# Kernel optimization log

Measured on AMD Instinct MI355X. Metric: run time of the kernel, lower is better.

Reference implementation:

```python
import jax, jax.numpy as jnp
import numpy as np

B, T, DIM = 4, 2048, 2048
H = 16
Q_LORA, KV_LORA = 1536, 512
ROPE_D, NOPE_D, V_D = 64, 128, 128
Q_HEAD_D = NOPE_D + ROPE_D  # 192
EPS = 1e-6
ROPE_THETA = 500000.0


def rmsnorm(x, w):
    xf = x.astype(jnp.float32)
    rms = jax.lax.rsqrt(jnp.mean(xf * xf, axis=-1, keepdims=True) + EPS)
    return (xf * rms).astype(x.dtype) * w


def apply_rope(x, cos, sin):
    # x: (B,T,H,d); cos/sin: (T,d//2). Complex mult on interleaved pairs.
    d = x.shape[-1]
    xp = x.reshape(*x.shape[:-1], d // 2, 2)
    x0, x1 = xp[..., 0], xp[..., 1]
    c = cos[None, :, None, :]
    s = sin[None, :, None, :]
    o0 = x0 * c - x1 * s
    o1 = x0 * s + x1 * c
    return jnp.stack([o0, o1], axis=-1).reshape(x.shape)


def setup_inputs() -> dict:
    key = jax.random.key(0)
    ks = jax.random.split(key, 8)
    x = jax.random.normal(ks[0], (B, T, DIM), dtype=jnp.float32)
    # RoPE freqs as in standard precompute_freqs_cis
    inv_freq = 1.0 / (ROPE_THETA ** (np.arange(0, ROPE_D, 2, dtype=np.float32) / ROPE_D))
    t = np.arange(T, dtype=np.float32)
    ang = np.outer(t, inv_freq)  # (T, 32)
    freqs_cos = jnp.asarray(np.cos(ang))
    freqs_sin = jnp.asarray(np.sin(ang))
    # causal additive mask (1,1,T,T)
    mask = jnp.where(jnp.tril(jnp.ones((T, T), dtype=bool)), 0.0, -1e9).astype(jnp.float32)[None, None]
    sc = lambda fan_in: 1.0 / np.sqrt(fan_in)
    q_down_w = jax.random.normal(ks[1], (Q_LORA, DIM), dtype=jnp.float32) * sc(DIM)
    q_norm_w = jnp.ones((Q_LORA,), dtype=jnp.float32)
    q_up_nope_w = jax.random.normal(ks[2], (H * NOPE_D, Q_LORA), dtype=jnp.float32) * sc(Q_LORA)
    q_up_rope_w = jax.random.normal(ks[3], (H * ROPE_D, Q_LORA), dtype=jnp.float32) * sc(Q_LORA)
    kv_down_w = jax.random.normal(ks[4], (KV_LORA + ROPE_D, DIM), dtype=jnp.float32) * sc(DIM)
    kv_norm_w = jnp.ones((KV_LORA,), dtype=jnp.float32)
    kv_up_w = jax.random.normal(ks[5], (H * (NOPE_D + V_D), KV_LORA), dtype=jnp.float32) * sc(KV_LORA)
    wo_w = jax.random.normal(ks[6], (DIM, H * V_D), dtype=jnp.float32) * sc(H * V_D)
    return {"x": x, "freqs_cos": freqs_cos, "freqs_sin": freqs_sin, "mask": mask,
            "q_down_w": q_down_w, "q_norm_w": q_norm_w, "q_up_nope_w": q_up_nope_w,
            "q_up_rope_w": q_up_rope_w, "kv_down_w": kv_down_w, "kv_norm_w": kv_norm_w,
            "kv_up_w": kv_up_w, "wo_w": wo_w}


def reference(x, freqs_cos, freqs_sin, mask, q_down_w, q_norm_w, q_up_nope_w,
              q_up_rope_w, kv_down_w, kv_norm_w, kv_up_w, wo_w):
    b, t, _ = x.shape
    # Q path: low-rank down -> RMSNorm -> nope/rope up projections
    c_q = rmsnorm(x @ q_down_w.T, q_norm_w)                      # (B,T,q_lora)
    q_nope = (c_q @ q_up_nope_w.T).reshape(b, t, H, NOPE_D)
    q_rope = (c_q @ q_up_rope_w.T).reshape(b, t, H, ROPE_D)
    q_rope = apply_rope(q_rope, freqs_cos, freqs_sin)
    q = jnp.concatenate([q_nope, q_rope], axis=-1)               # (B,T,H,192)
    # KV path: shared low-rank latent + per-sequence rope key
    kv_raw = x @ kv_down_w.T                                     # (B,T,512+64)
    c_kv = kv_raw[..., :KV_LORA]
    k_rope = kv_raw[..., KV_LORA:][:, :, None, :]                # (B,T,1,64)
    k_rope = apply_rope(k_rope, freqs_cos, freqs_sin)
    k_rope = jnp.broadcast_to(k_rope, (b, t, H, ROPE_D))
    kv = (rmsnorm(c_kv, kv_norm_w) @ kv_up_w.T).reshape(b, t, H, NOPE_D + V_D)
    k_nope = kv[..., :NOPE_D]
    v = kv[..., NOPE_D:]                                         # (B,T,H,128)
    k = jnp.concatenate([k_nope, k_rope], axis=-1)               # (B,T,H,192)
    scale = Q_HEAD_D ** -0.5
    attn = jnp.einsum('bthd,bshd->bhts', q, k) * scale + mask    # (B,H,T,T)
    attn = jax.nn.softmax(attn, axis=-1)
    out = jnp.einsum('bhts,bshd->bthd', attn, v).reshape(b, t, H * V_D)
    return out @ wo_w.T
```

## Files before the change

### kernel.cpp

```cpp
#include <hip/hip_runtime.h>

#define BB 4
#define TT 2048
#define HH 16
#define ROWS (BB*TT)

typedef unsigned short u16;
typedef __bf16 bf16x8 __attribute__((ext_vector_type(8)));
typedef float f32x4 __attribute__((ext_vector_type(4)));
typedef u16 u16x8 __attribute__((ext_vector_type(8)));
typedef u16 u16x4 __attribute__((ext_vector_type(4)));

__device__ __forceinline__ u16 f2bf(float f) {
  unsigned u = __float_as_uint(f);
  u += 0x7fffu + ((u >> 16) & 1u);
  return (u16)(u >> 16);
}
__device__ __forceinline__ float bf2f(u16 h) {
  return __uint_as_float(((unsigned)h) << 16);
}

__device__ __forceinline__ void gload_lds16(const u16* g, u16* l) {
  __builtin_amdgcn_global_load_lds((const __attribute__((address_space(1))) void*)g,
                                   (__attribute__((address_space(3))) void*)l, 16, 0, 0);
}

__global__ __launch_bounds__(256) void cast_bf16(const float* __restrict__ in,
                                                 u16* __restrict__ out,
                                                 long n, float scale) {
  long i = ((long)blockIdx.x * 256 + threadIdx.x) * 4;
  long stride = (long)gridDim.x * 1024;
  for (; i < n; i += stride) {
    float4 v = *(const float4*)(in + i);
    u16x4 o = { f2bf(v.x*scale), f2bf(v.y*scale), f2bf(v.z*scale), f2bf(v.w*scale) };
    *(u16x4*)(out + i) = o;
  }
}

__global__ __launch_bounds__(256) void cast_pad(const float* __restrict__ in,
                                                u16* __restrict__ out,
                                                long n_in, long n_total) {
  long i = ((long)blockIdx.x * 256 + threadIdx.x) * 4;
  long stride = (long)gridDim.x * 1024;
  for (; i < n_total; i += stride) {
    u16x4 o;
    if (i + 3 < n_in) {
      float4 v = *(const float4*)(in + i);
      o = (u16x4){ f2bf(v.x), f2bf(v.y), f2bf(v.z), f2bf(v.w) };
    } else {
#pragma unroll
      for (int e = 0; e < 4; ++e) o[e] = (i + e < n_in) ? f2bf(in[i+e]) : (u16)0;
    }
    *(u16x4*)(out + i) = o;
  }
}

template<int OUT_BF16>
__global__ __launch_bounds__(512, 2) void gemm256(const u16* __restrict__ A,
                                                  const u16* __restrict__ Bm,
                                                  void* __restrict__ Cv,
                                                  int M, int N, int K, int lda) {
  __shared__ __align__(16) u16 lds[65536];
  const int tid = threadIdx.x;
  const int lane = tid & 63, wid = tid >> 6;
  const int wm = (wid >> 2) * 128;
  const int wn = (wid & 3) * 64;

  const int nx = gridDim.x;
  int id = blockIdx.y * nx + blockIdx.x;
  const int cpx = (nx * gridDim.y) >> 3;
  id = (id & 7) * cpx + (id >> 3);
  const int m0 = (id / nx) * 256;
  const int n0 = (id % nx) * 256;

  const int NT = K >> 6;

  f32x4 acc[8][4] = {};

  auto stage = [&](int kt, int d) {
#pragma unroll
    for (int j = 0; j < 4; ++j) {
      int c = j*512 + tid;
      int row = c >> 3;
      int colb = (c & 7) << 4;
      int srcb = colb ^ ((row & 7) << 4);
      const u16* ga = (const u16*)((const char*)A + ((long)(m0 + row) * lda + kt*64) * 2 + srcb);
      gload_lds16(ga, (u16*)((char*)lds + d*65536 + c*16));
      const u16* gb = (const u16*)((const char*)Bm + ((long)(n0 + row) * K + kt*64) * 2 + srcb);
      gload_lds16(gb, (u16*)((char*)lds + d*65536 + 32768 + c*16));
    }
  };

  stage(0, 0);
  stage(1, 1);

  const int lr = lane & 15;
  const int kb = (lane >> 4) << 4;

  for (int kt = 0; kt < NT; ++kt) {
    const int cur = kt & 1;
    if (kt + 1 < NT) asm volatile("s_waitcnt vmcnt(8)" ::: "memory");
    else             asm volatile("s_waitcnt vmcnt(0)" ::: "memory");
    __builtin_amdgcn_s_barrier();
    __builtin_amdgcn_sched_barrier(0);

    const char* Ab = (const char*)lds + cur*65536;
    const char* Bb = Ab + 32768;
#pragma unroll
    for (int qd = 0; qd < 4; ++qd) {
      const int mb = (qd >> 1) * 4;
      const int nb = (qd & 1) * 2;
      bf16x8 af[4][2], bf[2][2];
#pragma unroll
      for (int i = 0; i < 4; ++i) {
        int r = wm + (mb + i)*16 + lr;
#pragma unroll
        for (int ks = 0; ks < 2; ++ks)
          af[i][ks] = *(const bf16x8*)(Ab + r*128 + ((ks*64 + kb) ^ ((r & 7) << 4)));
      }
#pragma unroll
      for (int i = 0; i < 2; ++i) {
        int r = wn + (nb + i)*16 + lr;
#pragma unroll
        for (int ks = 0; ks < 2; ++ks)
          bf[i][ks] = *(const bf16x8*)(Bb + r*128 + ((ks*64 + kb) ^ ((r & 7) << 4)));
      }
      __builtin_amdgcn_s_setprio(1);
#pragma unroll
      for (int ks = 0; ks < 2; ++ks)
#pragma unroll
        for (int i = 0; i < 4; ++i)
#pragma unroll
          for (int j = 0; j < 2; ++j)
            acc[mb+i][nb+j] = __builtin_amdgcn_mfma_f32_16x16x32_bf16(af[i][ks], bf[j][ks], acc[mb+i][nb+j], 0, 0, 0);
      __builtin_amdgcn_s_setprio(0);
    }
    __builtin_amdgcn_sched_barrier(0);
    __builtin_amdgcn_s_barrier();
    if (kt + 2 < NT) stage(kt + 2, cur);
  }

  const int orow = (lane >> 4) << 2;
  const int ocol = lane & 15;
#pragma unroll
  for (int mf = 0; mf < 8; ++mf)
#pragma unroll
    for (int nf = 0; nf < 4; ++nf) {
      long rbase = (long)(m0 + wm + mf*16 + orow);
      int col = n0 + wn + nf*16 + ocol;
#pragma unroll
      for (int rr = 0; rr < 4; ++rr) {
        if (OUT_BF16) ((u16*)Cv)[(rbase + rr) * (long)N + col] = f2bf(acc[mf][nf][rr]);
        else          ((float*)Cv)[(rbase + rr) * (long)N + col] = acc[mf][nf][rr];
      }
    }
}

__global__ __launch_bounds__(256) void rmsnorm_bf(const u16* __restrict__ in, int istride,
                                                  const float* __restrict__ w,
                                                  u16* __restrict__ out, int ostride,
                                                  int N, float invn) {
  const long row = blockIdx.x;
  const u16* x = in + row * istride;
  u16* y = out + row * ostride;
  float ss = 0.f;
  for (int i = threadIdx.x * 8; i < N; i += 2048) {
    u16x8 v = *(const u16x8*)(x + i);
#pragma unroll
    for (int e = 0; e < 8; ++e) { float f = bf2f(v[e]); ss += f*f; }
  }
#pragma unroll
  for (int off = 32; off > 0; off >>= 1) ss += __shfl_down(ss, off);
  __shared__ float red[4];
  if ((threadIdx.x & 63) == 0) red[threadIdx.x >> 6] = ss;
  __syncthreads();
  float rms = rsqrtf((red[0]+red[1]+red[2]+red[3]) * invn + 1e-6f);
  for (int i = threadIdx.x * 8; i < N; i += 2048) {
    u16x8 v = *(const u16x8*)(x + i);
    u16x8 o;
#pragma unroll
    for (int e = 0; e < 8; ++e) o[e] = f2bf(bf2f(v[e]) * rms * w[i+e]);
    *(u16x8*)(y + i) = o;
  }
}

__global__ __launch_bounds__(256) void rope_qk(u16* __restrict__ qcat,
                                               const u16* __restrict__ dk,
                                               u16* __restrict__ Kr,
                                               const float* __restrict__ cosb,
                                               const float* __restrict__ sinb) {
  const int row = blockIdx.x;
  const int t = row & (TT-1);
  const float sc = 0.10411754661f;
  for (int p = threadIdx.x; p < 512; p += 256) {
    int h = p >> 5, i = p & 31;
    long base = (long)row*3072 + 2048 + h*64 + 2*i;
    float x0 = bf2f(qcat[base]), x1 = bf2f(qcat[base+1]);
    float c = cosb[t*32 + i], s = sinb[t*32 + i];
    qcat[base]   = f2bf((x0*c - x1*s)*sc);
    qcat[base+1] = f2bf((x0*s + x1*c)*sc);
  }
  if (threadIdx.x < 32) {
    int i = threadIdx.x;
    float x0 = bf2f(dk[(long)row*2304 + 2048 + 2*i]);
    float x1 = bf2f(dk[(long)row*2304 + 2048 + 2*i + 1]);
    float c = cosb[t*32 + i], s = sinb[t*32 + i];
    Kr[row*64 + 2*i]   = f2bf(x0*c - x1*s);
    Kr[row*64 + 2*i+1] = f2bf(x0*s + x1*c);
  }
}

__global__ __launch_bounds__(256) void transpose_v(const u16* __restrict__ kvb,
                                                   u16* __restrict__ Vt) {
  __shared__ u16 tile[64][136];
  const int bh = blockIdx.y;
  const int t0 = blockIdx.x << 6;
  const int tid = threadIdx.x;
  const long rowbase = (long)(bh >> 4) * TT + t0;
#pragma unroll
  for (int it = 0; it < 4; ++it) {
    int r = it*16 + (tid >> 4);
    int c = (tid & 15) << 3;
    u16x8 v = *(const u16x8*)(kvb + (rowbase + r) * 4096 + (bh & 15) * 256 + 128 + c);
#pragma unroll
    for (int e = 0; e < 8; ++e) tile[r][c+e] = v[e];
  }
  __syncthreads();
#pragma unroll
  for (int it = 0; it < 4; ++it) {
    int d = it*32 + (tid >> 3);
    int tc = (tid & 7) << 3;
    u16x8 o;
#pragma unroll
    for (int e = 0; e < 8; ++e) o[e] = tile[tc+e][d];
    *(u16x8*)(Vt + ((long)bh * 128 + d) * TT + t0 + tc) = o;
  }
}

__global__ __launch_bounds__(512) void flash_attn9(const u16* __restrict__ qcat,
                                                   const u16* __restrict__ kvb,
                                                   const u16* __restrict__ kr,
                                                   const u16* __restrict__ Vt,
                                                   u16* __restrict__ O) {
  __shared__ __align__(16) u16 lds[36864];
  const int bid = blockIdx.x;
  const int u = bid & 255, sl = bid >> 8;
  const int a = u >> 6;
  const int bh = u & 63;
  const int qt = sl ? a : (7 - a);
  const int b = bh >> 4, h = bh & 15;
  const int wid = threadIdx.x >> 6, lane = threadIdx.x & 63;
  const int q0 = qt*256 + wid*32;
  const long browq = (long)b * TT + q0;
  const long browk = (long)b * TT;
  const int l16 = lane >> 4;
  const int l8  = lane >> 3;
  const int lx16   = (lane & 15) * 16;
  const int lx8_16 = (lane & 7) * 16;
  const int co = l16 * 16;

  bf16x8 qf[2][6];
#pragma unroll
  for (int f = 0; f < 2; ++f) {
    long row = browq + f*16 + (lane & 15);
#pragma unroll
    for (int ks = 0; ks < 4; ++ks)
      qf[f][ks] = *(const bf16x8*)(qcat + row * 3072 + h*128 + ks*32 + l16 * 8);
#pragma unroll
    for (int ks = 0; ks < 2; ++ks)
      qf[f][4+ks] = *(const bf16x8*)(qcat + row * 3072 + 2048 + h*64 + ks*32 + l16 * 8);
  }

  bf16x8 vones;
#pragma unroll
  for (int e = 0; e < 8; ++e) vones[e] = (__bf16)1.0f;

  f32x4 oacc[2][8] = {};
  f32x4 lsum[2] = {};

  u16* pw = lds + 20480 + wid * 2048;

  const int nIter = 4*qt + 4;
  for (int it = 0; it < nIter; ++it) {
    const int s0 = it * 64;
#pragma unroll
    for (int j = 0; j < 2; ++j) {
      int c = j*8 + wid;
      int r = c*4 + l16;
      int cb = lx16 ^ ((r & 7) << 4);
      const u16* src = (const u16*)((const char*)kvb + (browk + s0 + r) * 8192 + h * 512 + cb);
      gload_lds16(src, lds + c*512);
    }
    {
      int c = wid;
      int r = c*8 + l8;
      int cb = lx8_16 ^ ((r & 7) << 4);
      const u16* src = (const u16*)((const char*)kr + (browk + s0 + r) * 128 + cb);
      gload_lds16(src, lds + 8192 + c*512);
    }
#pragma unroll
    for (int j = 0; j < 2; ++j) {
      int c = j*8 + wid;
      int d = c*8 + l8;
      int cb = lx8_16 ^ ((d & 7) << 4);
      const u16* src = (const u16*)((const char*)Vt + ((long)bh*128 + d) * (TT*2) + (long)s0*2 + cb);
      gload_lds16(src, lds + 12288 + c*512);
    }
    __syncthreads();

    const bool skip0 = s0 > q0 + 15;
    const bool skip1 = s0 > q0 + 31;
    if (!skip0 || !skip1) {
      __builtin_amdgcn_s_setprio(1);
      f32x4 sacc[2][4] = {};
#pragma unroll
      for (int nt = 0; nt < 4; ++nt) {
        const int r = nt*16 + (lane & 15);
        const int swz = (r & 7) << 4;
        bf16x8 kf[6];
#pragma unroll
        for (int ks = 0; ks < 4; ++ks)
          kf[ks] = *(const bf16x8*)((const char*)lds + r*256 + ((ks*64 + co) ^ swz));
#pragma unroll
        for (int ks = 0; ks < 2; ++ks)
          kf[4+ks] = *(const bf16x8*)((const char*)lds + 16384 + r*128 + ((ks*64 + co) ^ swz));
        if (!skip0) {
#pragma unroll
          for (int ks = 0; ks < 6; ++ks)
            sacc[0][nt] = __builtin_amdgcn_mfma_f32_16x16x32_bf16(qf[0][ks], kf[ks], sacc[0][nt], 0, 0, 0);
        }
        if (!skip1) {
#pragma unroll
          for (int ks = 0; ks < 6; ++ks)
            sacc[1][nt] = __builtin_amdgcn_mfma_f32_16x16x32_bf16(qf[1][ks], kf[ks], sacc[1][nt], 0, 0, 0);
        }
      }
#pragma unroll
      for (int f = 0; f < 2; ++f) {
        const bool skipf = f ? skip1 : skip0;
        if (skipf) continue;
        const int qmin = q0 + f*16;
        const int qb = qmin + (l16 << 2);
        if (s0 + 63 > qmin) {
#pragma unroll
          for (int nt = 0; nt < 4; ++nt) {
            int sc = s0 + nt*16 + (lane & 15);
#pragma unroll
            for (int rr = 0; rr < 4; ++rr)
              if (sc > qb + rr) sacc[f][nt][rr] = -1e30f;
          }
        }
        const int lb2 = (lane & 15) * 2;
#pragma unroll
        for (int rr = 0; rr < 4; ++rr) {
          float p0 = exp2f(sacc[f][0][rr] - 16.f);
          float p1 = exp2f(sacc[f][1][rr] - 16.f);
          float p2 = exp2f(sacc[f][2][rr] - 16.f);
          float p3 = exp2f(sacc[f][3][rr] - 16.f);
          const int prow = f*16 + (l16 << 2) + rr;
          const int sw = (prow & 7) << 4;
          char* pb = (char*)pw + prow*128;
          *(u16*)(pb + ((     lb2) ^ sw)) = f2bf(p0);
          *(u16*)(pb + (( 32 + lb2) ^ sw)) = f2bf(p1);
          *(u16*)(pb + (( 64 + lb2) ^ sw)) = f2bf(p2);
          *(u16*)(pb + (( 96 + lb2) ^ sw)) = f2bf(p3);
        }
      }
#pragma unroll
      for (int ks = 0; ks < 2; ++ks) {
        const int cb = ks*64 + co;
        bf16x8 vf[8];
#pragma unroll
        for (int vt = 0; vt < 8; ++vt) {
          int row = vt*16 + (lane & 15);
          vf[vt] = *(const bf16x8*)((const char*)lds + 24576 + row*128 + (cb ^ ((row & 7) << 4)));
        }
#pragma unroll
        for (int f = 0; f < 2; ++f) {
          if (f ? skip1 : skip0) continue;
          int prow = f*16 + (lane & 15);
          bf16x8 pa = *(const bf16x8*)((const char*)pw + prow*128 + (cb ^ ((prow & 7) << 4)));
          lsum[f] = __builtin_amdgcn_mfma_f32_16x16x32_bf16(pa, vones, lsum[f], 0, 0, 0);
#pragma unroll
          for (int vt = 0; vt < 8; ++vt)
            oacc[f][vt] = __builtin_amdgcn_mfma_f32_16x16x32_bf16(pa, vf[vt], oacc[f][vt], 0, 0, 0);
        }
      }
      __builtin_amdgcn_s_setprio(0);
    }
    __syncthreads();
  }

#pragma unroll
  for (int f = 0; f < 2; ++f) {
    float inv[4];
#pragma unroll
    for (int rr = 0; rr < 4; ++rr) inv[rr] = 1.f / lsum[f][rr];
#pragma unroll
    for (int vt = 0; vt < 8; ++vt)
#pragma unroll
      for (int rr = 0; rr < 4; ++rr) {
        long row = browq + f*16 + (l16 << 2) + rr;
        int col = h*128 + vt*16 + (lane & 15);
        O[row * 2048 + col] = f2bf(oacc[f][vt][rr] * inv[rr]);
      }
  }
}

static inline long minl(long a, long b) { return a < b ? a : b; }
static inline int cgrid(long n) { return (int)minl((n/4 + 255)/256, 4096L); }

extern "C" void kernel_launch(void* const* d_in, const int* in_sizes, int n_in,
                              void* d_out, int out_size, void* d_ws, size_t ws_size,
                              hipStream_t stream) {
  const float* x    = (const float*)d_in[0];
  const float* fcos = (const float*)d_in[1];
  const float* fsin = (const float*)d_in[2];
  const float* qdw  = (const float*)d_in[4];
  const float* qnw  = (const float*)d_in[5];
  const float* qunw = (const float*)d_in[6];
  const float* qurw = (const float*)d_in[7];
  const float* kvdw = (const float*)d_in[8];
  const float* kvnw = (const float*)d_in[9];
  const float* kvuw = (const float*)d_in[10];
  const float* wow  = (const float*)d_in[11];
  float* out = (float*)d_out;

  char* p = (char*)d_ws;
  auto alloc = [&](size_t bytes) { char* r = p; p += (bytes + 255) & ~(size_t)255; return r; };

  u16* xb   = (u16*)alloc((size_t)ROWS*2048*2);
  u16* wdc  = (u16*)alloc((size_t)2304*2048*2);
  u16* wuc  = (u16*)alloc((size_t)3072*1536*2);
  u16* wkvu = (u16*)alloc((size_t)4096*512*2);
  u16* wwo  = (u16*)alloc((size_t)2048*2048*2);
  u16* dk   = (u16*)alloc((size_t)ROWS*2304*2);
  u16* qcat = (u16*)alloc((size_t)ROWS*3072*2);
  u16* kvb  = (u16*)alloc((size_t)ROWS*4096*2);
  u16* kro  = (u16*)alloc((size_t)ROWS*64*2);

  u16* Vt = dk;
  u16* Ob = xb;

  const float QSC_E = 0.10411754661f;

  cast_bf16<<<cgrid((long)ROWS*2048), 256, 0, stream>>>(x, xb, (long)ROWS*2048, 1.f);
  cast_bf16<<<cgrid(1536L*2048), 256, 0, stream>>>(qdw, wdc, 1536L*2048, 1.f);
  cast_pad<<<cgrid(768L*2048), 256, 0, stream>>>(kvdw, wdc + 1536L*2048, 576L*2048, 768L*2048);
  cast_bf16<<<cgrid(2048L*1536), 256, 0, stream>>>(qunw, wuc, 2048L*1536, QSC_E);
  cast_bf16<<<cgrid(1024L*1536), 256, 0, stream>>>(qurw, wuc + 2048L*1536, 1024L*1536, 1.f);
  cast_bf16<<<cgrid(4096L*512), 256, 0, stream>>>(kvuw, wkvu, 4096L*512, 1.f);
  cast_bf16<<<cgrid(2048L*2048), 256, 0, stream>>>(wow, wwo, 2048L*2048, 1.f);

  gemm256<1><<<dim3(9, 32), 512, 0, stream>>>(xb, wdc, dk, ROWS, 2304, 2048, 2048);
  rmsnorm_bf<<<ROWS, 256, 0, stream>>>(dk, 2304, qnw, dk, 2304, 1536, 1.f/1536.f);
  rmsnorm_bf<<<ROWS, 256, 0, stream>>>(dk + 1536, 2304, kvnw, dk + 1536, 2304, 512, 1.f/512.f);
  gemm256<1><<<dim3(12, 32), 512, 0, stream>>>(dk, wuc, qcat, ROWS, 3072, 1536, 2304);
  gemm256<1><<<dim3(16, 32), 512, 0, stream>>>(dk + 1536, wkvu, kvb, ROWS, 4096, 512, 2304);
  rope_qk<<<ROWS, 256, 0, stream>>>(qcat, dk, kro, fcos, fsin);
  transpose_v<<<dim3(TT/64, BB*HH), 256, 0, stream>>>(kvb, Vt);
  flash_attn9<<<512, 512, 0, stream>>>(qcat, kvb, kro, Vt, Ob);
  gemm256<0><<<dim3(8, 32), 512, 0, stream>>>(Ob, wwo, out, ROWS, 2048, 2048, 2048);
}
```

Measured before the change: 575.0 us.

## Fuse weight casts, merge rmsnorm with k-rope, write V transposed from GEMM epilogue

Six weight-cast launches are merged into one multi-segment cast kernel. The two rmsnorms and the k-rope step are merged into a single per-row kernel. The kv-up GEMM now has an epilogue mode that writes k_nope to a compact buffer and V directly in transposed layout, which removes the separate transpose kernel and the full kvb round trip. Costs are fewer launches and less memory traffic, in exchange for 8-byte strided V stores in the epilogue and branchy segment selection in the cast kernel.

```diff
diff --git a/kernel.cpp b/kernel.cpp
--- a/kernel.cpp
+++ b/kernel.cpp
@@ -26,39 +26,57 @@
 }
 
 __global__ __launch_bounds__(256) void cast_bf16(const float* __restrict__ in,
-                                                 u16* __restrict__ out,
-                                                 long n, float scale) {
+                                                 u16* __restrict__ out, long n) {
   long i = ((long)blockIdx.x * 256 + threadIdx.x) * 4;
   long stride = (long)gridDim.x * 1024;
   for (; i < n; i += stride) {
     float4 v = *(const float4*)(in + i);
-    u16x4 o = { f2bf(v.x*scale), f2bf(v.y*scale), f2bf(v.z*scale), f2bf(v.w*scale) };
+    u16x4 o = { f2bf(v.x), f2bf(v.y), f2bf(v.z), f2bf(v.w) };
     *(u16x4*)(out + i) = o;
   }
 }
 
-__global__ __launch_bounds__(256) void cast_pad(const float* __restrict__ in,
-                                                u16* __restrict__ out,
-                                                long n_in, long n_total) {
+__global__ __launch_bounds__(256) void cast_weights(const float* __restrict__ qdw,
+                                                    const float* __restrict__ kvdw,
+                                                    const float* __restrict__ qunw,
+                                                    const float* __restrict__ qurw,
+                                                    const float* __restrict__ kvuw,
+                                                    const float* __restrict__ wow,
+                                                    u16* __restrict__ wdc,
+                                                    u16* __restrict__ wuc,
+                                                    u16* __restrict__ wkvu,
+                                                    u16* __restrict__ wwo,
+                                                    float qsc) {
+  const long s0 = 1536L*2048, s1 = 768L*2048, s2 = 2048L*1536,
+             s3 = 1024L*1536, s4 = 4096L*512,  s5 = 2048L*2048;
+  const long total = s0+s1+s2+s3+s4+s5;
   long i = ((long)blockIdx.x * 256 + threadIdx.x) * 4;
   long stride = (long)gridDim.x * 1024;
-  for (; i < n_total; i += stride) {
+  for (; i < total; i += stride) {
+    long off = i; const float* src; u16* dst; float sc = 1.f; long lim = -1;
+    if (off < s0)               { src = qdw;  dst = wdc; }
+    else if ((off -= s0) < s1)  { src = kvdw; dst = wdc + s0; lim = 576L*2048; }
+    else if ((off -= s1) < s2)  { src = qunw; dst = wuc; sc = qsc; }
+    else if ((off -= s2) < s3)  { src = qurw; dst = wuc + s2; }
+    else if ((off -= s3) < s4)  { src = kvuw; dst = wkvu; }
+    else { off -= s4;             src = wow;  dst = wwo; }
     u16x4 o;
-    if (i + 3 < n_in) {
-      float4 v = *(const float4*)(in + i);
-      o = (u16x4){ f2bf(v.x), f2bf(v.y), f2bf(v.z), f2bf(v.w) };
+    if (lim < 0 || off + 3 < lim) {
+      float4 v = *(const float4*)(src + off);
+      o = (u16x4){ f2bf(v.x*sc), f2bf(v.y*sc), f2bf(v.z*sc), f2bf(v.w*sc) };
     } else {
 #pragma unroll
-      for (int e = 0; e < 4; ++e) o[e] = (i + e < n_in) ? f2bf(in[i+e]) : (u16)0;
-    }
-    *(u16x4*)(out + i) = o;
-  }
-}
-
-template<int OUT_BF16>
+      for (int e = 0; e < 4; ++e) o[e] = (off + e < lim) ? f2bf(src[off+e]*sc) : (u16)0;
+    }
+    *(u16x4*)(dst + off) = o;
+  }
+}
+
+template<int MODE>
 __global__ __launch_bounds__(512, 2) void gemm256(const u16* __restrict__ A,
                                                   const u16* __restrict__ Bm,
                                                   void* __restrict__ Cv,
+                                                  u16* __restrict__ Vt,
                                                   int M, int N, int K, int lda) {
   __shared__ __align__(16) u16 lds[65536];
   const int tid = threadIdx.x;
@@ -148,47 +166,84 @@
     for (int nf = 0; nf < 4; ++nf) {
       long rbase = (long)(m0 + wm + mf*16 + orow);
       int col = n0 + wn + nf*16 + ocol;
-#pragma unroll
-      for (int rr = 0; rr < 4; ++rr) {
-        if (OUT_BF16) ((u16*)Cv)[(rbase + rr) * (long)N + col] = f2bf(acc[mf][nf][rr]);
-        else          ((float*)Cv)[(rbase + rr) * (long)N + col] = acc[mf][nf][rr];
-      }
-    }
-}
-
-__global__ __launch_bounds__(256) void rmsnorm_bf(const u16* __restrict__ in, int istride,
-                                                  const float* __restrict__ w,
-                                                  u16* __restrict__ out, int ostride,
-                                                  int N, float invn) {
+      if (MODE == 0) {
+#pragma unroll
+        for (int rr = 0; rr < 4; ++rr)
+          ((float*)Cv)[(rbase + rr) * (long)N + col] = acc[mf][nf][rr];
+      } else if (MODE == 1) {
+#pragma unroll
+        for (int rr = 0; rr < 4; ++rr)
+          ((u16*)Cv)[(rbase + rr) * (long)N + col] = f2bf(acc[mf][nf][rr]);
+      } else {
+        int h = col >> 8, inner = col & 255;
+        if (inner < 128) {
+#pragma unroll
+          for (int rr = 0; rr < 4; ++rr)
+            ((u16*)Cv)[(rbase + rr) * 2048L + h*128 + inner] = f2bf(acc[mf][nf][rr]);
+        } else {
+          int bb = (int)(rbase >> 11);
+          int t  = (int)(rbase & 2047);
+          long vo = ((long)(bb*16 + h) * 128 + (inner - 128)) * 2048 + t;
+          u16x4 o = { f2bf(acc[mf][nf][0]), f2bf(acc[mf][nf][1]),
+                      f2bf(acc[mf][nf][2]), f2bf(acc[mf][nf][3]) };
+          *(u16x4*)(Vt + vo) = o;
+        }
+      }
+    }
+}
+
+__global__ __launch_bounds__(256) void rms_rope_dk(u16* __restrict__ dk,
+                                                   const float* __restrict__ qnw,
+                                                   const float* __restrict__ kvnw,
+                                                   u16* __restrict__ Kr,
+                                                   const float* __restrict__ cosb,
+                                                   const float* __restrict__ sinb) {
   const long row = blockIdx.x;
-  const u16* x = in + row * istride;
-  u16* y = out + row * ostride;
-  float ss = 0.f;
-  for (int i = threadIdx.x * 8; i < N; i += 2048) {
-    u16x8 v = *(const u16x8*)(x + i);
-#pragma unroll
-    for (int e = 0; e < 8; ++e) { float f = bf2f(v[e]); ss += f*f; }
-  }
-#pragma unroll
-  for (int off = 32; off > 0; off >>= 1) ss += __shfl_down(ss, off);
-  __shared__ float red[4];
-  if ((threadIdx.x & 63) == 0) red[threadIdx.x >> 6] = ss;
+  u16* x = dk + row * 2304;
+  const int i = threadIdx.x * 8;
+  float sq = 0.f, sk = 0.f;
+  u16x8 v = *(const u16x8*)(x + i);
+  {
+    float s = 0.f;
+#pragma unroll
+    for (int e = 0; e < 8; ++e) { float f = bf2f(v[e]); s += f*f; }
+    if (i < 1536) sq = s; else sk = s;
+  }
+#pragma unroll
+  for (int off = 32; off > 0; off >>= 1) {
+    sq += __shfl_down(sq, off);
+    sk += __shfl_down(sk, off);
+  }
+  __shared__ float redq[4], redk[4];
+  if ((threadIdx.x & 63) == 0) {
+    redq[threadIdx.x >> 6] = sq;
+    redk[threadIdx.x >> 6] = sk;
+  }
   __syncthreads();
-  float rms = rsqrtf((red[0]+red[1]+red[2]+red[3]) * invn + 1e-6f);
-  for (int i = threadIdx.x * 8; i < N; i += 2048) {
-    u16x8 v = *(const u16x8*)(x + i);
+  float rq = rsqrtf((redq[0]+redq[1]+redq[2]+redq[3]) * (1.f/1536.f) + 1e-6f);
+  float rk = rsqrtf((redk[0]+redk[1]+redk[2]+redk[3]) * (1.f/512.f) + 1e-6f);
+  {
+    float r = (i < 1536) ? rq : rk;
+    const float* w = (i < 1536) ? (qnw + i) : (kvnw + (i - 1536));
     u16x8 o;
 #pragma unroll
-    for (int e = 0; e < 8; ++e) o[e] = f2bf(bf2f(v[e]) * rms * w[i+e]);
-    *(u16x8*)(y + i) = o;
-  }
-}
-
-__global__ __launch_bounds__(256) void rope_qk(u16* __restrict__ qcat,
-                                               const u16* __restrict__ dk,
-                                               u16* __restrict__ Kr,
-                                               const float* __restrict__ cosb,
-                                               const float* __restrict__ sinb) {
+    for (int e = 0; e < 8; ++e) o[e] = f2bf(bf2f(v[e]) * r * w[e]);
+    *(u16x8*)(x + i) = o;
+  }
+  if (threadIdx.x < 32) {
+    const int t = (int)(row & (TT-1));
+    int ii = threadIdx.x;
+    float x0 = bf2f(x[2048 + 2*ii]);
+    float x1 = bf2f(x[2048 + 2*ii + 1]);
+    float c = cosb[t*32 + ii], s = sinb[t*32 + ii];
+    Kr[row*64 + 2*ii]     = f2bf(x0*c - x1*s);
+    Kr[row*64 + 2*ii + 1] = f2bf(x0*s + x1*c);
+  }
+}
+
+__global__ __launch_bounds__(256) void rope_q(u16* __restrict__ qcat,
+                                              const float* __restrict__ cosb,
+                                              const float* __restrict__ sinb) {
   const int row = blockIdx.x;
   const int t = row & (TT-1);
   const float sc = 0.10411754661f;
@@ -200,45 +255,10 @@
     qcat[base]   = f2bf((x0*c - x1*s)*sc);
     qcat[base+1] = f2bf((x0*s + x1*c)*sc);
   }
-  if (threadIdx.x < 32) {
-    int i = threadIdx.x;
-    float x0 = bf2f(dk[(long)row*2304 + 2048 + 2*i]);
-    float x1 = bf2f(dk[(long)row*2304 + 2048 + 2*i + 1]);
-    float c = cosb[t*32 + i], s = sinb[t*32 + i];
-    Kr[row*64 + 2*i]   = f2bf(x0*c - x1*s);
-    Kr[row*64 + 2*i+1] = f2bf(x0*s + x1*c);
-  }
-}
-
-__global__ __launch_bounds__(256) void transpose_v(const u16* __restrict__ kvb,
-                                                   u16* __restrict__ Vt) {
-  __shared__ u16 tile[64][136];
-  const int bh = blockIdx.y;
-  const int t0 = blockIdx.x << 6;
-  const int tid = threadIdx.x;
-  const long rowbase = (long)(bh >> 4) * TT + t0;
-#pragma unroll
-  for (int it = 0; it < 4; ++it) {
-    int r = it*16 + (tid >> 4);
-    int c = (tid & 15) << 3;
-    u16x8 v = *(const u16x8*)(kvb + (rowbase + r) * 4096 + (bh & 15) * 256 + 128 + c);
-#pragma unroll
-    for (int e = 0; e < 8; ++e) tile[r][c+e] = v[e];
-  }
-  __syncthreads();
-#pragma unroll
-  for (int it = 0; it < 4; ++it) {
-    int d = it*32 + (tid >> 3);
-    int tc = (tid & 7) << 3;
-    u16x8 o;
-#pragma unroll
-    for (int e = 0; e < 8; ++e) o[e] = tile[tc+e][d];
-    *(u16x8*)(Vt + ((long)bh * 128 + d) * TT + t0 + tc) = o;
-  }
 }
 
 __global__ __launch_bounds__(512) void flash_attn9(const u16* __restrict__ qcat,
-                                                   const u16* __restrict__ kvb,
+                                                   const u16* __restrict__ kn,
                                                    const u16* __restrict__ kr,
                                                    const u16* __restrict__ Vt,
                                                    u16* __restrict__ O) {
@@ -288,7 +308,7 @@
       int c = j*8 + wid;
       int r = c*4 + l16;
       int cb = lx16 ^ ((r & 7) << 4);
-      const u16* src = (const u16*)((const char*)kvb + (browk + s0 + r) * 8192 + h * 512 + cb);
+      const u16* src = (const u16*)((const char*)kn + (browk + s0 + r) * 4096 + h * 256 + cb);
       gload_lds16(src, lds + c*512);
     }
     {
@@ -436,29 +456,23 @@
   u16* wwo  = (u16*)alloc((size_t)2048*2048*2);
   u16* dk   = (u16*)alloc((size_t)ROWS*2304*2);
   u16* qcat = (u16*)alloc((size_t)ROWS*3072*2);
-  u16* kvb  = (u16*)alloc((size_t)ROWS*4096*2);
+  u16* kn   = (u16*)alloc((size_t)ROWS*2048*2);
+  u16* Vt   = (u16*)alloc((size_t)ROWS*2048*2);
   u16* kro  = (u16*)alloc((size_t)ROWS*64*2);
 
-  u16* Vt = dk;
   u16* Ob = xb;
 
   const float QSC_E = 0.10411754661f;
 
-  cast_bf16<<<cgrid((long)ROWS*2048), 256, 0, stream>>>(x, xb, (long)ROWS*2048, 1.f);
-  cast_bf16<<<cgrid(1536L*2048), 256, 0, stream>>>(qdw, wdc, 1536L*2048, 1.f);
-  cast_pad<<<cgrid(768L*2048), 256, 0, stream>>>(kvdw, wdc + 1536L*2048, 576L*2048, 768L*2048);
-  cast_bf16<<<cgrid(2048L*1536), 256, 0, stream>>>(qunw, wuc, 2048L*1536, QSC_E);
-  cast_bf16<<<cgrid(1024L*1536), 256, 0, stream>>>(qurw, wuc + 2048L*1536, 1024L*1536, 1.f);
-  cast_bf16<<<cgrid(4096L*512), 256, 0, stream>>>(kvuw, wkvu, 4096L*512, 1.f);
-  cast_bf16<<<cgrid(2048L*2048), 256, 0, stream>>>(wow, wwo, 2048L*2048, 1.f);
-
-  gemm256<1><<<dim3(9, 32), 512, 0, stream>>>(xb, wdc, dk, ROWS, 2304, 2048, 2048);
-  rmsnorm_bf<<<ROWS, 256, 0, stream>>>(dk, 2304, qnw, dk, 2304, 1536, 1.f/1536.f);
-  rmsnorm_bf<<<ROWS, 256, 0, stream>>>(dk + 1536, 2304, kvnw, dk + 1536, 2304, 512, 1.f/512.f);
-  gemm256<1><<<dim3(12, 32), 512, 0, stream>>>(dk, wuc, qcat, ROWS, 3072, 1536, 2304);
-  gemm256<1><<<dim3(16, 32), 512, 0, stream>>>(dk + 1536, wkvu, kvb, ROWS, 4096, 512, 2304);
-  rope_qk<<<ROWS, 256, 0, stream>>>(qcat, dk, kro, fcos, fsin);
-  transpose_v<<<dim3(TT/64, BB*HH), 256, 0, stream>>>(kvb, Vt);
-  flash_attn9<<<512, 512, 0, stream>>>(qcat, kvb, kro, Vt, Ob);
-  gemm256<0><<<dim3(8, 32), 512, 0, stream>>>(Ob, wwo, out, ROWS, 2048, 2048, 2048);
-}
+  cast_bf16<<<cgrid((long)ROWS*2048), 256, 0, stream>>>(x, xb, (long)ROWS*2048);
+  cast_weights<<<4096, 256, 0, stream>>>(qdw, kvdw, qunw, qurw, kvuw, wow,
+                                         wdc, wuc, wkvu, wwo, QSC_E);
+
+  gemm256<1><<<dim3(9, 32), 512, 0, stream>>>(xb, wdc, dk, nullptr, ROWS, 2304, 2048, 2048);
+  rms_rope_dk<<<ROWS, 256, 0, stream>>>(dk, qnw, kvnw, kro, fcos, fsin);
+  gemm256<1><<<dim3(12, 32), 512, 0, stream>>>(dk, wuc, qcat, nullptr, ROWS, 3072, 1536, 2304);
+  gemm256<2><<<dim3(16, 32), 512, 0, stream>>>(dk + 1536, wkvu, kn, Vt, ROWS, 4096, 512, 2304);
+  rope_q<<<ROWS, 256, 0, stream>>>(qcat, fcos, fsin);
+  flash_attn9<<<512, 512, 0, stream>>>(qcat, kn, kro, Vt, Ob);
+  gemm256<0><<<dim3(8, 32), 512, 0, stream>>>(Ob, wwo, out, nullptr, ROWS, 2048, 2048, 2048);
+}
```

New measurement: 550.2 us. 1.05x faster.
